# Kernel optimization log

Measured on AMD Instinct MI355X. Metric: run time of the kernel, lower is better.

## Reference

```python
import jax, jax.numpy as jnp
import numpy as np


def _lstm_dir(x, mask, Wi, Wh, b, reverse):
    """One direction of an LSTM layer with per-path length masking.
    x: [P,T,D], mask: [P,T] bool (True where t < length).
    Returns (outputs [P,T,H], final hidden [P,H]).
    State freezes outside the valid region, so the final carry equals the
    hidden state at the last valid step (fwd: t=len-1; bwd: t=0), matching
    torch's per-sequence LSTM on the unpadded sequence."""
    P, T, D = x.shape
    H = Wh.shape[1]
    xs = jnp.swapaxes(x, 0, 1)      # [T,P,D]
    ms = jnp.swapaxes(mask, 0, 1)   # [T,P]
    if reverse:
        xs, ms = xs[::-1], ms[::-1]
    h0 = jnp.zeros((P, H), x.dtype)

    def step(carry, inp):
        h, c = carry
        xt, mt = inp
        z = xt @ Wi.T + h @ Wh.T + b          # [P,4H], torch gate order i,f,g,o
        i, f, g, o = jnp.split(z, 4, axis=-1)
        c_new = jax.nn.sigmoid(f) * c + jax.nn.sigmoid(i) * jnp.tanh(g)
        h_new = jax.nn.sigmoid(o) * jnp.tanh(c_new)
        m = mt[:, None]
        h = jnp.where(m, h_new, h)
        c = jnp.where(m, c_new, c)
        return (h, c), h

    (h_fin, _), hs = jax.lax.scan(step, (h0, h0), (xs, ms))
    if reverse:
        hs = hs[::-1]
    return jnp.swapaxes(hs, 0, 1), h_fin


def setup_inputs() -> dict:
    key = jax.random.key(0)
    N, E, F, H, P, T = 50000, 256, 64, 256, 512, 256
    s = 0.05
    ks = jax.random.split(key, 24)
    d = {}
    d['sequences'] = jax.random.randint(ks[0], (P, T), 0, N)
    d['lengths'] = jax.random.randint(ks[1], (P,), 1, T + 1)  # >=1 so all paths valid
    d['features'] = jax.random.normal(ks[2], (P, F), jnp.float32)
    d['node_embeddings'] = jax.random.normal(ks[3], (N, E), jnp.float32)
    d['num_paths'] = P
    # node_projection
    d['Wp'] = jax.random.normal(ks[4], (H, E), jnp.float32) * s
    d['bp'] = jnp.zeros((H,), jnp.float32)
    # LSTM layer 0 (input H), fwd/rev; b = b_ih + b_hh folded together
    d['Wi0f'] = jax.random.normal(ks[5], (4 * H, H), jnp.float32) * s
    d['Wh0f'] = jax.random.normal(ks[6], (4 * H, H), jnp.float32) * s
    d['b0f'] = jnp.zeros((4 * H,), jnp.float32)
    d['Wi0r'] = jax.random.normal(ks[7], (4 * H, H), jnp.float32) * s
    d['Wh0r'] = jax.random.normal(ks[8], (4 * H, H), jnp.float32) * s
    d['b0r'] = jnp.zeros((4 * H,), jnp.float32)
    # LSTM layer 1 (input 2H), fwd/rev
    d['Wi1f'] = jax.random.normal(ks[9], (4 * H, 2 * H), jnp.float32) * s
    d['Wh1f'] = jax.random.normal(ks[10], (4 * H, H), jnp.float32) * s
    d['b1f'] = jnp.zeros((4 * H,), jnp.float32)
    d['Wi1r'] = jax.random.normal(ks[11], (4 * H, 2 * H), jnp.float32) * s
    d['Wh1r'] = jax.random.normal(ks[12], (4 * H, H), jnp.float32) * s
    d['b1r'] = jnp.zeros((4 * H,), jnp.float32)
    # feature_projection
    d['Wf'] = jax.random.normal(ks[13], (H, F), jnp.float32) * s
    d['bf'] = jnp.zeros((H,), jnp.float32)
    # path_fusion (3H -> H)
    d['Wfus'] = jax.random.normal(ks[14], (H, 3 * H), jnp.float32) * s
    d['bfus'] = jnp.zeros((H,), jnp.float32)
    # attention_projection (H -> 1)
    d['Wa'] = jax.random.normal(ks[15], (1, H), jnp.float32) * s
    d['ba'] = jnp.zeros((1,), jnp.float32)
    # aggregation_mlp: 3H -> 2H -> H
    d['W1'] = jax.random.normal(ks[16], (2 * H, 3 * H), jnp.float32) * s
    d['b1'] = jnp.zeros((2 * H,), jnp.float32)
    d['W2'] = jax.random.normal(ks[17], (H, 2 * H), jnp.float32) * s
    d['b2'] = jnp.zeros((H,), jnp.float32)
    return d


def reference(sequences, lengths, features, node_embeddings, num_paths,
              Wp, bp,
              Wi0f, Wh0f, b0f, Wi0r, Wh0r, b0r,
              Wi1f, Wh1f, b1f, Wi1r, Wh1r, b1r,
              Wf, bf, Wfus, bfus, Wa, ba, W1, b1, W2, b2):
    P, T = sequences.shape
    # gather + node projection (eval mode: dropout off)
    x = node_embeddings[sequences] @ Wp.T + bp               # [P,T,H]
    mask = jnp.arange(T)[None, :] < lengths[:, None]         # [P,T]
    # BiLSTM layer 0
    o0f, _ = _lstm_dir(x, mask, Wi0f, Wh0f, b0f, reverse=False)
    o0r, _ = _lstm_dir(x, mask, Wi0r, Wh0r, b0r, reverse=True)
    o0 = jnp.concatenate([o0f, o0r], axis=-1)                # [P,T,2H]
    # BiLSTM layer 1: only final hidden states needed (h_n[-2], h_n[-1])
    _, h1f = _lstm_dir(o0, mask, Wi1f, Wh1f, b1f, reverse=False)
    _, h1r = _lstm_dir(o0, mask, Wi1r, Wh1r, b1r, reverse=True)
    path_lstm = jnp.concatenate([h1f, h1r], axis=-1)         # [P,2H]
    path_feat = features @ Wf.T + bf                         # [P,H]
    combined = jnp.concatenate([path_lstm, path_feat], axis=-1)
    path_emb = jax.nn.relu(combined @ Wfus.T + bfus)         # [P,H]
    # attention pooling over paths
    attn = jax.nn.softmax(path_emb @ Wa.T + ba, axis=0)      # [P,1]
    weighted = (path_emb * attn).sum(axis=0, keepdims=True)  # [1,H]
    mean_p = path_emb.mean(axis=0, keepdims=True)
    max_p = path_emb.max(axis=0, keepdims=True)
    agg = jnp.concatenate([weighted, mean_p, max_p], axis=1)  # [1,3H]
    h = jax.nn.relu(agg @ W1.T + b1)
    return h @ W2.T + b2                                     # [1,H]
```

## Files before the change

kernel.cpp:

```cpp
#include <hip/hip_runtime.h>

typedef short bf8 __attribute__((ext_vector_type(8)));
typedef float f4  __attribute__((ext_vector_type(4)));
typedef int   i4  __attribute__((ext_vector_type(4)));

#define DEV static __device__ __forceinline__

DEV float bf2f(unsigned short u){ unsigned int x = ((unsigned int)u) << 16; float f; __builtin_memcpy(&f, &x, 4); return f; }
DEV unsigned short f2bf(float f){ unsigned int x; __builtin_memcpy(&x, &f, 4); unsigned int r = (x + 0x7fffu + ((x >> 16) & 1u)) >> 16; return (unsigned short)r; }
DEV float sigm(float z){ return 1.f / (1.f + __expf(-z)); }
DEV float tanh_fast(float z){ float e = __expf(2.f * z); return 1.f - 2.f / (e + 1.f); }

__global__ void k_cvt(const float* __restrict__ s, unsigned short* __restrict__ d, int n){
    int i = blockIdx.x * 256 + threadIdx.x;
    if (i < n) d[i] = f2bf(s[i]);
}

__global__ void k_cvt_t(const float* __restrict__ s, unsigned short* __restrict__ d){
    int e = blockIdx.x, h = threadIdx.x;
    d[e * 256 + h] = f2bf(s[h * 256 + e]);
}

__global__ void k_bias(const float* __restrict__ b0f, const float* __restrict__ Wi0f,
                       const float* __restrict__ b0r, const float* __restrict__ Wi0r,
                       const float* __restrict__ bp, float* __restrict__ bc){
    int g = blockIdx.x * 256 + threadIdx.x;
    const float* b = (g < 1024) ? b0f : b0r;
    const float* W = ((g < 1024) ? Wi0f : Wi0r) + (size_t)(g & 1023) * 256;
    float a = b[g & 1023];
    for (int k = 0; k < 256; ++k) a += W[k] * bp[k];
    bc[g] = a;
}

template<int K, int AMODE, bool OUTH>
__global__ __launch_bounds__(256)
void k_gemm(const unsigned short* __restrict__ A, const int* __restrict__ seq,
            const unsigned short* __restrict__ W, const float* __restrict__ bias,
            void* __restrict__ C, int N, int t0)
{
    __shared__ unsigned short Alds[128 * 32];
    __shared__ unsigned short Blds[128 * 32];
    const int tid = threadIdx.x, lane = tid & 63, wv = tid >> 6;
    const long m0 = (long)blockIdx.x * 128, n0 = (long)blockIdx.y * 128;

    const unsigned short* srcA[2]; const unsigned short* srcB[2]; int ldsOfs[2];
    #pragma unroll
    for (int q = 0; q < 2; ++q){
        int c = wv * 128 + q * 64 + lane;
        int r = c >> 2, kb = c & 3;
        int kg = kb ^ ((r >> 1) & 3);
        long m = m0 + r;
        long arow;
        if constexpr (AMODE == 0){
            arow = m;
        } else {
            long p = m >> 5; int ss = (int)(m & 31);
            int t = (AMODE == 2 || AMODE == 4) ? (t0 + ss) : (t0 - ss);
            arow = p * 256 + t;
            if constexpr (AMODE == 2 || AMODE == 3) arow = seq[arow];
        }
        srcA[q] = A + arow * K + kg * 8;
        srcB[q] = W + (n0 + r) * K + kg * 8;
        ldsOfs[q] = c * 8;
    }
    f4 acc[4][4] = {};
    const int ar = lane & 15, kq = lane >> 4;
    const int wm = (wv >> 1) * 64, wn = (wv & 1) * 64;

    for (int kk = 0; kk < K / 32; ++kk){
        i4 ra[2], rb[2];
        #pragma unroll
        for (int q = 0; q < 2; ++q){
            ra[q] = *(const i4*)(srcA[q] + kk * 32);
            rb[q] = *(const i4*)(srcB[q] + kk * 32);
        }
        __syncthreads();
        #pragma unroll
        for (int q = 0; q < 2; ++q){
            *(i4*)&Alds[ldsOfs[q]] = ra[q];
            *(i4*)&Blds[ldsOfs[q]] = rb[q];
        }
        __syncthreads();
        bf8 af[4], bfr[4];
        #pragma unroll
        for (int mt = 0; mt < 4; ++mt){
            int row = wm + mt * 16 + ar; int ph = kq ^ ((row >> 1) & 3);
            af[mt] = __builtin_bit_cast(bf8, *(const i4*)&Alds[row * 32 + ph * 8]);
        }
        #pragma unroll
        for (int nt = 0; nt < 4; ++nt){
            int row = wn + nt * 16 + ar; int ph = kq ^ ((row >> 1) & 3);
            bfr[nt] = __builtin_bit_cast(bf8, *(const i4*)&Blds[row * 32 + ph * 8]);
        }
        #pragma unroll
        for (int mt = 0; mt < 4; ++mt)
            #pragma unroll
            for (int nt = 0; nt < 4; ++nt)
                acc[mt][nt] = __builtin_amdgcn_mfma_f32_16x16x32_bf16(af[mt], bfr[nt], acc[mt][nt], 0, 0, 0);
    }
    #pragma unroll
    for (int nt = 0; nt < 4; ++nt){
        long n = n0 + wn + nt * 16 + ar;
        float bv = bias[n];
        #pragma unroll
        for (int mt = 0; mt < 4; ++mt){
            #pragma unroll
            for (int r = 0; r < 4; ++r){
                long m = m0 + wm + mt * 16 + kq * 4 + r;
                float v = acc[mt][nt][r] + bv;
                if (OUTH) ((_Float16*)C)[m * N + n] = (_Float16)v;
                else      ((unsigned short*)C)[m * N + n] = f2bf(v);
            }
        }
    }
}

template<int LAYER>
__global__ __launch_bounds__(256)
void k_step(int s, const unsigned short* __restrict__ Wh,
            const _Float16* __restrict__ zxF,
            const _Float16* __restrict__ zxR,
            unsigned short* __restrict__ o0,
            const unsigned short* __restrict__ hsR, unsigned short* __restrict__ hsW,
            float* __restrict__ cbuf,
            const int* __restrict__ lengths)
{
    __shared__ unsigned short Wlds[128 * 256];
    const int tid = threadIdx.x, lane = tid & 63, wv = tid >> 6;
    const int pt = blockIdx.x, jc = blockIdx.y, dir = blockIdx.z;
    const int t = dir ? 255 - s : s;
    const int tprev = dir ? t + 1 : t - 1;

    if (s > 0){
        for (int c = tid; c < 4096; c += 256){
            int r = c >> 5, kb = c & 31;
            int kg = kb ^ (r & 7);
            int wrow = (r >> 5) * 256 + jc * 32 + (r & 31);
            *(i4*)&Wlds[c * 8] = *(const i4*)&Wh[((size_t)(dir * 1024 + wrow)) * 256 + kg * 8];
        }
    }
    __syncthreads();

    const int ar = lane & 15, kq = lane >> 4;
    const int p0 = pt * 64 + wv * 16 + ar;
    f4 acc[8] = {};
    if (s > 0){
        bf8 af[8];
        const unsigned short* hp;
        if constexpr (LAYER == 0) hp = o0 + ((size_t)(p0 * 256 + tprev)) * 512 + dir * 256;
        else                      hp = hsR + ((size_t)(dir * 512 + p0)) * 256;
        #pragma unroll
        for (int k0 = 0; k0 < 8; ++k0)
            af[k0] = __builtin_bit_cast(bf8, *(const i4*)&hp[k0 * 32 + kq * 8]);
        #pragma unroll
        for (int nt = 0; nt < 8; ++nt){
            int row = nt * 16 + ar;
            #pragma unroll
            for (int k0 = 0; k0 < 8; ++k0){
                int ph = (k0 * 4 + kq) ^ (row & 7);
                bf8 b = __builtin_bit_cast(bf8, *(const i4*)&Wlds[row * 256 + ph * 8]);
                acc[nt] = __builtin_amdgcn_mfma_f32_16x16x32_bf16(af[k0], b, acc[nt], 0, 0, 0);
            }
        }
    }
    const _Float16* zb = dir ? zxR : zxF;
    const int ss = s & 31;
    #pragma unroll
    for (int sub = 0; sub < 2; ++sub){
        const int hcol = jc * 32 + sub * 16 + ar;
        #pragma unroll
        for (int r = 0; r < 4; ++r){
            const int path = pt * 64 + wv * 16 + kq * 4 + r;
            const size_t zofs = (((size_t)path << 5) + ss) * 1024 + hcol;
            float zi = acc[0 + sub][r] + (float)zb[zofs];
            float zf = acc[2 + sub][r] + (float)zb[zofs + 256];
            float zg = acc[4 + sub][r] + (float)zb[zofs + 512];
            float zo = acc[6 + sub][r] + (float)zb[zofs + 768];
            const bool m = t < lengths[path];
            float* cp = cbuf + ((size_t)(dir * 512 + path)) * 256 + hcol;
            float cold = *cp;
            float ig = sigm(zi), fg = sigm(zf), gg = tanh_fast(zg), og = sigm(zo);
            float cn = fg * cold + ig * gg;
            float hn = og * tanh_fast(cn);
            float hold = 0.f;
            if (s > 0){
                if constexpr (LAYER == 0) hold = bf2f(o0[((size_t)path * 256 + tprev) * 512 + dir * 256 + hcol]);
                else                      hold = bf2f(hsR[((size_t)(dir * 512 + path)) * 256 + hcol]);
            }
            if (m) *cp = cn;
            float ho = m ? hn : hold;
            if constexpr (LAYER == 0) o0[((size_t)path * 256 + t) * 512 + dir * 256 + hcol] = f2bf(ho);
            else                      hsW[((size_t)(dir * 512 + path)) * 256 + hcol] = f2bf(ho);
        }
    }
}

__global__ __launch_bounds__(256)
void k_fuse(const unsigned short* __restrict__ hsF,
            const float* __restrict__ features, const float* __restrict__ Wf, const float* __restrict__ bfv,
            const float* __restrict__ Wfus, const float* __restrict__ bfus,
            const float* __restrict__ Wa, const float* __restrict__ ba,
            float* __restrict__ pe, float* __restrict__ scores)
{
    __shared__ float comb[768];
    __shared__ float fl[64];
    __shared__ float red[256];
    const int p = blockIdx.x, tid = threadIdx.x;
    comb[tid]       = bf2f(hsF[(size_t)(0 * 512 + p) * 256 + tid]);
    comb[256 + tid] = bf2f(hsF[(size_t)(1 * 512 + p) * 256 + tid]);
    if (tid < 64) fl[tid] = features[p * 64 + tid];
    __syncthreads();
    float pf = bfv[tid];
    #pragma unroll 4
    for (int k = 0; k < 64; ++k) pf += fl[k] * Wf[tid * 64 + k];
    comb[512 + tid] = pf;
    __syncthreads();
    float a = bfus[tid];
    #pragma unroll 4
    for (int k = 0; k < 768; ++k) a += comb[k] * Wfus[tid * 768 + k];
    float pev = fmaxf(a, 0.f);
    pe[(size_t)p * 256 + tid] = pev;
    red[tid] = pev * Wa[tid];
    __syncthreads();
    for (int ofs = 128; ofs > 0; ofs >>= 1){
        if (tid < ofs) red[tid] += red[tid + ofs];
        __syncthreads();
    }
    if (tid == 0) scores[p] = red[0] + ba[0];
}

__global__ __launch_bounds__(512)
void k_head(const float* __restrict__ pe, const float* __restrict__ scores,
            const float* __restrict__ W1, const float* __restrict__ b1,
            const float* __restrict__ W2, const float* __restrict__ b2,
            float* __restrict__ out)
{
    __shared__ float att[512];
    __shared__ float red[512];
    __shared__ float agg[768];
    __shared__ float h1[512];
    const int tid = threadIdx.x;
    float s = scores[tid];
    red[tid] = s; __syncthreads();
    for (int ofs = 256; ofs > 0; ofs >>= 1){ if (tid < ofs) red[tid] = fmaxf(red[tid], red[tid + ofs]); __syncthreads(); }
    float mx = red[0]; __syncthreads();
    float e = __expf(s - mx);
    red[tid] = e; __syncthreads();
    for (int ofs = 256; ofs > 0; ofs >>= 1){ if (tid < ofs) red[tid] += red[tid + ofs]; __syncthreads(); }
    float sum = red[0]; __syncthreads();
    att[tid] = e / sum;
    __syncthreads();
    if (tid < 256){
        float w = 0.f, sm = 0.f, mxv = -1e30f;
        for (int p = 0; p < 512; ++p){
            float v = pe[(size_t)p * 256 + tid];
            w += att[p] * v; sm += v; mxv = fmaxf(mxv, v);
        }
        agg[tid] = w; agg[256 + tid] = sm * (1.f / 512.f); agg[512 + tid] = mxv;
    }
    __syncthreads();
    float hv = b1[tid];
    #pragma unroll 4
    for (int k = 0; k < 768; ++k) hv += agg[k] * W1[tid * 768 + k];
    hv = fmaxf(hv, 0.f);
    h1[tid] = hv;
    __syncthreads();
    if (tid < 256){
        float o = b2[tid];
        #pragma unroll 4
        for (int k = 0; k < 512; ++k) o += h1[k] * W2[tid * 512 + k];
        out[tid] = o;
    }
}

extern "C" void kernel_launch(void* const* d_in, const int* in_sizes, int n_in,
                              void* d_out, int out_size, void* d_ws, size_t ws_size,
                              hipStream_t stream)
{
    const int*   seq  = (const int*)  d_in[0];
    const int*   len  = (const int*)  d_in[1];
    const float* feat = (const float*)d_in[2];
    const float* emb  = (const float*)d_in[3];
    const float* Wp   = (const float*)d_in[5];
    const float* bp   = (const float*)d_in[6];
    const float* Wi0f = (const float*)d_in[7];
    const float* Wh0f = (const float*)d_in[8];
    const float* b0f  = (const float*)d_in[9];
    const float* Wi0r = (const float*)d_in[10];
    const float* Wh0r = (const float*)d_in[11];
    const float* b0r  = (const float*)d_in[12];
    const float* Wi1f = (const float*)d_in[13];
    const float* Wh1f = (const float*)d_in[14];
    const float* b1f  = (const float*)d_in[15];
    const float* Wi1r = (const float*)d_in[16];
    const float* Wh1r = (const float*)d_in[17];
    const float* b1r  = (const float*)d_in[18];
    const float* Wf   = (const float*)d_in[19];
    const float* bfv  = (const float*)d_in[20];
    const float* Wfus = (const float*)d_in[21];
    const float* bfus = (const float*)d_in[22];
    const float* Wa   = (const float*)d_in[23];
    const float* ba   = (const float*)d_in[24];
    const float* W1   = (const float*)d_in[25];
    const float* b1   = (const float*)d_in[26];
    const float* W2   = (const float*)d_in[27];
    const float* b2   = (const float*)d_in[28];

    char* ws = (char*)d_ws;
    size_t o = 0;
    auto alloc = [&](size_t bytes)->char*{ char* r = ws + o; o += (bytes + 255) & ~(size_t)255; return r; };

    unsigned short* emb_bf = (unsigned short*)alloc(50000UL * 256 * 2);
    unsigned short* wpT    = (unsigned short*)alloc(256UL * 256 * 2);
    unsigned short* wi0b   = (unsigned short*)alloc(2048UL * 256 * 2);
    unsigned short* wc0    = (unsigned short*)alloc(2048UL * 256 * 2);
    float*          bc0    = (float*)        alloc(2048UL * 4);
    float*          zbias  = (float*)        alloc(256UL * 4);
    unsigned short* wi1b   = (unsigned short*)alloc(2048UL * 512 * 2);
    unsigned short* wh0b   = (unsigned short*)alloc(2048UL * 256 * 2);
    unsigned short* wh1b   = (unsigned short*)alloc(2048UL * 256 * 2);
    unsigned short* o0p    = (unsigned short*)alloc(131072UL * 512 * 2);
    _Float16*       zxF    = (_Float16*)     alloc(512UL * 32 * 1024 * 2);
    _Float16*       zxR    = (_Float16*)     alloc(512UL * 32 * 1024 * 2);
    float*          c0p    = (float*)        alloc(2UL * 512 * 256 * 4);
    float*          c1p    = (float*)        alloc(2UL * 512 * 256 * 4);
    unsigned short* hsA    = (unsigned short*)alloc(2UL * 512 * 256 * 2);
    unsigned short* hsB    = (unsigned short*)alloc(2UL * 512 * 256 * 2);
    float*          pe     = (float*)        alloc(512UL * 256 * 4);
    float*          scores = (float*)        alloc(512UL * 4);
    (void)in_sizes; (void)n_in; (void)out_size;
    if (o > ws_size) return;

    auto cvt = [&](const float* s, unsigned short* d, int n){
        k_cvt<<<(n + 255) / 256, 256, 0, stream>>>(s, d, n);
    };
    cvt(emb,  emb_bf, 50000 * 256);
    k_cvt_t<<<256, 256, 0, stream>>>(Wp, wpT);
    cvt(Wi0f, wi0b,              1024 * 256);
    cvt(Wi0r, wi0b + 1024 * 256, 1024 * 256);
    cvt(Wh0f, wh0b,              1024 * 256);
    cvt(Wh0r, wh0b + 1024 * 256, 1024 * 256);
    cvt(Wi1f, wi1b,              1024 * 512);
    cvt(Wi1r, wi1b + 1024 * 512, 1024 * 512);
    cvt(Wh1f, wh1b,              1024 * 256);
    cvt(Wh1r, wh1b + 1024 * 256, 1024 * 256);
    k_bias<<<8, 256, 0, stream>>>(b0f, Wi0f, b0r, Wi0r, bp, bc0);
    hipMemsetAsync(zbias, 0, 256 * 4, stream);
    hipMemsetAsync(c0p, 0, 2UL * 512 * 256 * 4, stream);
    hipMemsetAsync(c1p, 0, 2UL * 512 * 256 * 4, stream);

    k_gemm<256, 0, false><<<dim3(16, 2), 256, 0, stream>>>(wi0b, nullptr, wpT, zbias, wc0, 256, 0);

    for (int c = 0; c < 8; ++c){
        int s0 = c * 32;
        k_gemm<256, 2, true><<<dim3(128, 8), 256, 0, stream>>>(emb_bf, seq, wc0,              bc0,        zxF, 1024, s0);
        k_gemm<256, 3, true><<<dim3(128, 8), 256, 0, stream>>>(emb_bf, seq, wc0 + 1024 * 256, bc0 + 1024, zxR, 1024, 255 - s0);
        for (int s = s0; s < s0 + 32; ++s)
            k_step<0><<<dim3(8, 8, 2), 256, 0, stream>>>(s, wh0b, zxF, zxR, o0p, nullptr, nullptr, c0p, len);
    }
    for (int c = 0; c < 8; ++c){
        int s0 = c * 32;
        k_gemm<512, 4, true><<<dim3(128, 8), 256, 0, stream>>>(o0p, nullptr, wi1b,              b1f, zxF, 1024, s0);
        k_gemm<512, 5, true><<<dim3(128, 8), 256, 0, stream>>>(o0p, nullptr, wi1b + 1024 * 512, b1r, zxR, 1024, 255 - s0);
        for (int s = s0; s < s0 + 32; ++s)
            k_step<1><<<dim3(8, 8, 2), 256, 0, stream>>>(s, wh1b, zxF, zxR, nullptr,
                (s & 1) ? hsA : hsB, (s & 1) ? hsB : hsA, c1p, len);
    }
    k_fuse<<<512, 256, 0, stream>>>(hsB, feat, Wf, bfv, Wfus, bfus, Wa, ba, pe, scores);
    k_head<<<1, 512, 0, stream>>>(pe, scores, W1, b1, W2, b2, (float*)d_out);
}
```

Baseline: 6.195 ms.

## Replace per-step LSTM launches with persistent kernels using flag-based cross-block sync

```diff
diff --git a/kernel.cpp b/kernel.cpp
--- a/kernel.cpp
+++ b/kernel.cpp
@@ -10,10 +10,16 @@
 DEV unsigned short f2bf(float f){ unsigned int x; __builtin_memcpy(&x, &f, 4); unsigned int r = (x + 0x7fffu + ((x >> 16) & 1u)) >> 16; return (unsigned short)r; }
 DEV float sigm(float z){ return 1.f / (1.f + __expf(-z)); }
 DEV float tanh_fast(float z){ float e = __expf(2.f * z); return 1.f - 2.f / (e + 1.f); }
+DEV bf8 ld16(const unsigned short* p){ return __builtin_bit_cast(bf8, *(const i4*)p); }
 
 __global__ void k_cvt(const float* __restrict__ s, unsigned short* __restrict__ d, int n){
     int i = blockIdx.x * 256 + threadIdx.x;
     if (i < n) d[i] = f2bf(s[i]);
+}
+
+__global__ void k_zero(unsigned int* __restrict__ d, int n){
+    int i = blockIdx.x * 256 + threadIdx.x;
+    if (i < n) d[i] = 0u;
 }
 
 __global__ void k_cvt_t(const float* __restrict__ s, unsigned short* __restrict__ d){
@@ -32,65 +38,46 @@
     bc[g] = a;
 }
 
-template<int K, int AMODE, bool OUTH>
 __global__ __launch_bounds__(256)
-void k_gemm(const unsigned short* __restrict__ A, const int* __restrict__ seq,
-            const unsigned short* __restrict__ W, const float* __restrict__ bias,
-            void* __restrict__ C, int N, int t0)
-{
+void k_gemm(const unsigned short* __restrict__ A, const unsigned short* __restrict__ W,
+            const float* __restrict__ bias, unsigned short* __restrict__ C, int N)
+{
+    const int K = 256;
     __shared__ unsigned short Alds[128 * 32];
     __shared__ unsigned short Blds[128 * 32];
     const int tid = threadIdx.x, lane = tid & 63, wv = tid >> 6;
     const long m0 = (long)blockIdx.x * 128, n0 = (long)blockIdx.y * 128;
-
     const unsigned short* srcA[2]; const unsigned short* srcB[2]; int ldsOfs[2];
     #pragma unroll
     for (int q = 0; q < 2; ++q){
         int c = wv * 128 + q * 64 + lane;
         int r = c >> 2, kb = c & 3;
         int kg = kb ^ ((r >> 1) & 3);
-        long m = m0 + r;
-        long arow;
-        if constexpr (AMODE == 0){
-            arow = m;
-        } else {
-            long p = m >> 5; int ss = (int)(m & 31);
-            int t = (AMODE == 2 || AMODE == 4) ? (t0 + ss) : (t0 - ss);
-            arow = p * 256 + t;
-            if constexpr (AMODE == 2 || AMODE == 3) arow = seq[arow];
-        }
-        srcA[q] = A + arow * K + kg * 8;
+        srcA[q] = A + (m0 + r) * K + kg * 8;
         srcB[q] = W + (n0 + r) * K + kg * 8;
         ldsOfs[q] = c * 8;
     }
     f4 acc[4][4] = {};
     const int ar = lane & 15, kq = lane >> 4;
     const int wm = (wv >> 1) * 64, wn = (wv & 1) * 64;
-
     for (int kk = 0; kk < K / 32; ++kk){
         i4 ra[2], rb[2];
         #pragma unroll
-        for (int q = 0; q < 2; ++q){
-            ra[q] = *(const i4*)(srcA[q] + kk * 32);
-            rb[q] = *(const i4*)(srcB[q] + kk * 32);
-        }
+        for (int q = 0; q < 2; ++q){ ra[q] = *(const i4*)(srcA[q] + kk * 32); rb[q] = *(const i4*)(srcB[q] + kk * 32); }
         __syncthreads();
         #pragma unroll
-        for (int q = 0; q < 2; ++q){
-            *(i4*)&Alds[ldsOfs[q]] = ra[q];
-            *(i4*)&Blds[ldsOfs[q]] = rb[q];
-        }
+        for (int q = 0; q < 2; ++q){ *(i4*)&Alds[ldsOfs[q]] = ra[q]; *(i4*)&Blds[ldsOfs[q]] = rb[q]; }
         __syncthreads();
         bf8 af[4], bfr[4];
         #pragma unroll
         for (int mt = 0; mt < 4; ++mt){
             int row = wm + mt * 16 + ar; int ph = kq ^ ((row >> 1) & 3);
-            af[mt] = __builtin_bit_cast(bf8, *(const i4*)&Alds[row * 32 + ph * 8]);
+            af[mt] = ld16(&Alds[row * 32 + ph * 8]);
         }
         #pragma unroll
         for (int nt = 0; nt < 4; ++nt){
             int row = wn + nt * 16 + ar; int ph = kq ^ ((row >> 1) & 3);
-            bfr[nt] = __builtin_bit_cast(bf8, *(const i4*)&Blds[row * 32 + ph * 8]);
+            bfr[nt] = ld16(&Blds[row * 32 + ph * 8]);
         }
         #pragma unroll
         for (int mt = 0; mt < 4; ++mt)
@@ -103,100 +90,146 @@
         long n = n0 + wn + nt * 16 + ar;
         float bv = bias[n];
         #pragma unroll
-        for (int mt = 0; mt < 4; ++mt){
+        for (int mt = 0; mt < 4; ++mt)
             #pragma unroll
             for (int r = 0; r < 4; ++r){
                 long m = m0 + wm + mt * 16 + kq * 4 + r;
-                float v = acc[mt][nt][r] + bv;
-                if (OUTH) ((_Float16*)C)[m * N + n] = (_Float16)v;
-                else      ((unsigned short*)C)[m * N + n] = f2bf(v);
-            }
-        }
+                C[m * N + n] = f2bf(acc[mt][nt][r] + bv);
+            }
     }
 }
 
 template<int LAYER>
+__global__ __launch_bounds__(256, 1)
+void k_persist(const unsigned short* __restrict__ Whw,
+               const unsigned short* __restrict__ Wxw,
+               const float* __restrict__ bias0,
+               const float* __restrict__ bias1,
+               const unsigned short* __restrict__ xsrc,
+               const int* __restrict__ seq,
+               const int* __restrict__ lengths,
+               unsigned short* __restrict__ o0,
+               unsigned short* __restrict__ hbuf,
+               unsigned int* __restrict__ flags)
+{
+    constexpr int XK = LAYER ? 512 : 256;
+    const int tid = threadIdx.x, lane = tid & 63, wv = tid >> 6;
+    const int b = blockIdx.x;
+    const int g = b & 15, jc = b >> 4;
+    const int pt = g >> 1, dir = g & 1;
+    const int ph = wv >> 1, gh = wv & 1;
+    const int pbase = pt * 64 + ph * 32;
+    const int hcbase = jc * 32 + gh * 16;
+    const int ar = lane & 15, kq = lane >> 4;
+    unsigned int* myflag = flags + g * 256;
+
+    bf8 whf[4][8], wxf[4][XK / 32];
+    #pragma unroll
+    for (int nt = 0; nt < 4; ++nt){
+        const int wrow = nt * 256 + hcbase + ar;
+        const unsigned short* wh = Whw + (size_t)(dir * 1024 + wrow) * 256 + kq * 8;
+        const unsigned short* wx = Wxw + (size_t)(dir * 1024 + wrow) * XK + kq * 8;
+        #pragma unroll
+        for (int k0 = 0; k0 < 8; ++k0) whf[nt][k0] = ld16(wh + k0 * 32);
+        #pragma unroll
+        for (int k0 = 0; k0 < XK / 32; ++k0) wxf[nt][k0] = ld16(wx + k0 * 32);
+    }
+    const int hcol = hcbase + ar;
+    const float* bb = dir ? bias1 : bias0;
+    const float bI = bb[hcol], bF = bb[256 + hcol], bG = bb[512 + hcol], bO = bb[768 + hcol];
+    int len_[2][4];
+    #pragma unroll
+    for (int mt = 0; mt < 2; ++mt)
+        #pragma unroll
+        for (int r = 0; r < 4; ++r) len_[mt][r] = lengths[pbase + mt * 16 + kq * 4 + r];
+    float cst[2][4] = {}, hst[2][4] = {};
+
+    for (int s = 0; s < 256; ++s){
+        const int t = dir ? 255 - s : s;
+        f4 acc[2][4] = {};
+        {
+            const unsigned short* xb[2];
+            #pragma unroll
+            for (int mt = 0; mt < 2; ++mt){
+                const int pa = pbase + mt * 16 + ar;
+                if constexpr (LAYER == 0){
+                    int e = seq[pa * 256 + t];
+                    xb[mt] = xsrc + (size_t)e * 256 + kq * 8;
+                } else {
+                    xb[mt] = xsrc + ((size_t)pa * 256 + t) * 512 + kq * 8;
+                }
+            }
+            #pragma unroll
+            for (int k0 = 0; k0 < XK / 32; ++k0){
+                bf8 a0 = ld16(xb[0] + k0 * 32);
+                bf8 a1 = ld16(xb[1] + k0 * 32);
+                #pragma unroll
+                for (int nt = 0; nt < 4; ++nt){
+                    acc[0][nt] = __builtin_amdgcn_mfma_f32_16x16x32_bf16(a0, wxf[nt][k0], acc[0][nt], 0, 0, 0);
+                    acc[1][nt] = __builtin_amdgcn_mfma_f32_16x16x32_bf16(a1, wxf[nt][k0], acc[1][nt], 0, 0, 0);
+                }
+            }
+        }
+        if (s > 0){
+            if (lane == 0){
+                unsigned int guard = 0;
+                while (__hip_atomic_load(myflag + (s - 1), __ATOMIC_ACQUIRE, __HIP_MEMORY_SCOPE_SYSTEM) < 8u){
+                    if (++guard > 2000000u) break;
+                    __builtin_amdgcn_s_sleep(1);
+                }
+            }
+            __syncthreads();
+            __threadfence();
+            const int tprev = dir ? t + 1 : t - 1;
+            const unsigned short* hb[2];
+            #pragma unroll
+            for (int mt = 0; mt < 2; ++mt){
+                const int pa = pbase + mt * 16 + ar;
+                if constexpr (LAYER == 0)
+                    hb[mt] = o0 + ((size_t)pa * 256 + tprev) * 512 + dir * 256 + kq * 8;
+                else
+                    hb[mt] = hbuf + ((size_t)((dir * 2 + ((s - 1) & 1)) * 512) + pa) * 256 + kq * 8;
+            }
+            #pragma unroll
+            for (int k0 = 0; k0 < 8; ++k0){
+                bf8 a0 = ld16(hb[0] + k0 * 32);
+                bf8 a1 = ld16(hb[1] + k0 * 32);
+                #pragma unroll
+                for (int nt = 0; nt < 4; ++nt){
+                    acc[0][nt] = __builtin_amdgcn_mfma_f32_16x16x32_bf16(a0, whf[nt][k0], acc[0][nt], 0, 0, 0);
+                    acc[1][nt] = __builtin_amdgcn_mfma_f32_16x16x32_bf16(a1, whf[nt][k0], acc[1][nt], 0, 0, 0);
+                }
+            }
+        }
+        #pragma unroll
+        for (int mt = 0; mt < 2; ++mt){
+            #pragma unroll
+            for (int r = 0; r < 4; ++r){
+                float zi = acc[mt][0][r] + bI;
+                float zf = acc[mt][1][r] + bF;
+                float zg = acc[mt][2][r] + bG;
+                float zo = acc[mt][3][r] + bO;
+                const int pa = pbase + mt * 16 + kq * 4 + r;
+                const bool m = t < len_[mt][r];
+                float cn = sigm(zf) * cst[mt][r] + sigm(zi) * tanh_fast(zg);
+                float hn = sigm(zo) * tanh_fast(cn);
+                if (m){ cst[mt][r] = cn; hst[mt][r] = hn; }
+                const unsigned short hb16 = f2bf(hst[mt][r]);
+                if constexpr (LAYER == 0)
+                    o0[((size_t)pa * 256 + t) * 512 + dir * 256 + hcol] = hb16;
+                else
+                    hbuf[((size_t)((dir * 2 + (s & 1)) * 512) + pa) * 256 + hcol] = hb16;
+            }
+        }
+        __threadfence();
+        __syncthreads();
+        if (tid == 0)
+            __hip_atomic_fetch_add(myflag + s, 1u, __ATOMIC_RELEASE, __HIP_MEMORY_SCOPE_SYSTEM);
+    }
+}
+
 __global__ __launch_bounds__(256)
-void k_step(int s, const unsigned short* __restrict__ Wh,
-            const _Float16* __restrict__ zxF,
-            const _Float16* __restrict__ zxR,
-            unsigned short* __restrict__ o0,
-            const unsigned short* __restrict__ hsR, unsigned short* __restrict__ hsW,
-            float* __restrict__ cbuf,
-            const int* __restrict__ lengths)
-{
-    __shared__ unsigned short Wlds[128 * 256];
-    const int tid = threadIdx.x, lane = tid & 63, wv = tid >> 6;
-    const int pt = blockIdx.x, jc = blockIdx.y, dir = blockIdx.z;
-    const int t = dir ? 255 - s : s;
-    const int tprev = dir ? t + 1 : t - 1;
-
-    if (s > 0){
-        for (int c = tid; c < 4096; c += 256){
-            int r = c >> 5, kb = c & 31;
-            int kg = kb ^ (r & 7);
-            int wrow = (r >> 5) * 256 + jc * 32 + (r & 31);
-            *(i4*)&Wlds[c * 8] = *(const i4*)&Wh[((size_t)(dir * 1024 + wrow)) * 256 + kg * 8];
-        }
-    }
-    __syncthreads();
-
-    const int ar = lane & 15, kq = lane >> 4;
-    const int p0 = pt * 64 + wv * 16 + ar;
-    f4 acc[8] = {};
-    if (s > 0){
-        bf8 af[8];
-        const unsigned short* hp;
-        if constexpr (LAYER == 0) hp = o0 + ((size_t)(p0 * 256 + tprev)) * 512 + dir * 256;
-        else                      hp = hsR + ((size_t)(dir * 512 + p0)) * 256;
-        #pragma unroll
-        for (int k0 = 0; k0 < 8; ++k0)
-            af[k0] = __builtin_bit_cast(bf8, *(const i4*)&hp[k0 * 32 + kq * 8]);
-        #pragma unroll
-        for (int nt = 0; nt < 8; ++nt){
-            int row = nt * 16 + ar;
-            #pragma unroll
-            for (int k0 = 0; k0 < 8; ++k0){
-                int ph = (k0 * 4 + kq) ^ (row & 7);
-                bf8 b = __builtin_bit_cast(bf8, *(const i4*)&Wlds[row * 256 + ph * 8]);
-                acc[nt] = __builtin_amdgcn_mfma_f32_16x16x32_bf16(af[k0], b, acc[nt], 0, 0, 0);
-            }
-        }
-    }
-    const _Float16* zb = dir ? zxR : zxF;
-    const int ss = s & 31;
-    #pragma unroll
-    for (int sub = 0; sub < 2; ++sub){
-        const int hcol = jc * 32 + sub * 16 + ar;
-        #pragma unroll
-        for (int r = 0; r < 4; ++r){
-            const int path = pt * 64 + wv * 16 + kq * 4 + r;
-            const size_t zofs = (((size_t)path << 5) + ss) * 1024 + hcol;
-            float zi = acc[0 + sub][r] + (float)zb[zofs];
-            float zf = acc[2 + sub][r] + (float)zb[zofs + 256];
-            float zg = acc[4 + sub][r] + (float)zb[zofs + 512];
-            float zo = acc[6 + sub][r] + (float)zb[zofs + 768];
-            const bool m = t < lengths[path];
-            float* cp = cbuf + ((size_t)(dir * 512 + path)) * 256 + hcol;
-            float cold = *cp;
-            float ig = sigm(zi), fg = sigm(zf), gg = tanh_fast(zg), og = sigm(zo);
-            float cn = fg * cold + ig * gg;
-            float hn = og * tanh_fast(cn);
-            float hold = 0.f;
-            if (s > 0){
-                if constexpr (LAYER == 0) hold = bf2f(o0[((size_t)path * 256 + tprev) * 512 + dir * 256 + hcol]);
-                else                      hold = bf2f(hsR[((size_t)(dir * 512 + path)) * 256 + hcol]);
-            }
-            if (m) *cp = cn;
-            float ho = m ? hn : hold;
-            if constexpr (LAYER == 0) o0[((size_t)path * 256 + t) * 512 + dir * 256 + hcol] = f2bf(ho);
-            else                      hsW[((size_t)(dir * 512 + path)) * 256 + hcol] = f2bf(ho);
-        }
-    }
-}
-
-__global__ __launch_bounds__(256)
-void k_fuse(const unsigned short* __restrict__ hsF,
+void k_fuse(const unsigned short* __restrict__ hbuf,
             const float* __restrict__ features, const float* __restrict__ Wf, const float* __restrict__ bfv,
             const float* __restrict__ Wfus, const float* __restrict__ bfus,
             const float* __restrict__ Wa, const float* __restrict__ ba,
@@ -206,8 +239,8 @@
     __shared__ float fl[64];
     __shared__ float red[256];
     const int p = blockIdx.x, tid = threadIdx.x;
-    comb[tid]       = bf2f(hsF[(size_t)(0 * 512 + p) * 256 + tid]);
-    comb[256 + tid] = bf2f(hsF[(size_t)(1 * 512 + p) * 256 + tid]);
+    comb[tid]       = bf2f(hbuf[((size_t)(0 * 2 + 1) * 512 + p) * 256 + tid]);
+    comb[256 + tid] = bf2f(hbuf[((size_t)(1 * 2 + 1) * 512 + p) * 256 + tid]);
     if (tid < 64) fl[tid] = features[p * 64 + tid];
     __syncthreads();
     float pf = bfv[tid];
@@ -320,12 +353,9 @@
     unsigned short* wh0b   = (unsigned short*)alloc(2048UL * 256 * 2);
     unsigned short* wh1b   = (unsigned short*)alloc(2048UL * 256 * 2);
     unsigned short* o0p    = (unsigned short*)alloc(131072UL * 512 * 2);
-    _Float16*       zxF    = (_Float16*)     alloc(512UL * 32 * 1024 * 2);
-    _Float16*       zxR    = (_Float16*)     alloc(512UL * 32 * 1024 * 2);
-    float*          c0p    = (float*)        alloc(2UL * 512 * 256 * 4);
-    float*          c1p    = (float*)        alloc(2UL * 512 * 256 * 4);
-    unsigned short* hsA    = (unsigned short*)alloc(2UL * 512 * 256 * 2);
-    unsigned short* hsB    = (unsigned short*)alloc(2UL * 512 * 256 * 2);
+    unsigned short* hbuf   = (unsigned short*)alloc(4UL * 512 * 256 * 2);
+    unsigned int*   flags0 = (unsigned int*) alloc(16UL * 256 * 4);
+    unsigned int*   flags1 = (unsigned int*) alloc(16UL * 256 * 4);
     float*          pe     = (float*)        alloc(512UL * 256 * 4);
     float*          scores = (float*)        alloc(512UL * 4);
     (void)in_sizes; (void)n_in; (void)out_size;
@@ -345,27 +375,15 @@
     cvt(Wh1f, wh1b,              1024 * 256);
     cvt(Wh1r, wh1b + 1024 * 256, 1024 * 256);
     k_bias<<<8, 256, 0, stream>>>(b0f, Wi0f, b0r, Wi0r, bp, bc0);
-    hipMemsetAsync(zbias, 0, 256 * 4, stream);
-    hipMemsetAsync(c0p, 0, 2UL * 512 * 256 * 4, stream);
-    hipMemsetAsync(c1p, 0, 2UL * 512 * 256 * 4, stream);
-
-    k_gemm<256, 0, false><<<dim3(16, 2), 256, 0, stream>>>(wi0b, nullptr, wpT, zbias, wc0, 256, 0);
-
-    for (int c = 0; c < 8; ++c){
-        int s0 = c * 32;
-        k_gemm<256, 2, true><<<dim3(128, 8), 256, 0, stream>>>(emb_bf, seq, wc0,              bc0,        zxF, 1024, s0);
-        k_gemm<256, 3, true><<<dim3(128, 8), 256, 0, stream>>>(emb_bf, seq, wc0 + 1024 * 256, bc0 + 1024, zxR, 1024, 255 - s0);
-        for (int s = s0; s < s0 + 32; ++s)
-            k_step<0><<<dim3(8, 8, 2), 256, 0, stream>>>(s, wh0b, zxF, zxR, o0p, nullptr, nullptr, c0p, len);
-    }
-    for (int c = 0; c < 8; ++c){
-        int s0 = c * 32;
-        k_gemm<512, 4, true><<<dim3(128, 8), 256, 0, stream>>>(o0p, nullptr, wi1b,              b1f, zxF, 1024, s0);
-        k_gemm<512, 5, true><<<dim3(128, 8), 256, 0, stream>>>(o0p, nullptr, wi1b + 1024 * 512, b1r, zxR, 1024, 255 - s0);
-        for (int s = s0; s < s0 + 32; ++s)
-            k_step<1><<<dim3(8, 8, 2), 256, 0, stream>>>(s, wh1b, zxF, zxR, nullptr,
-                (s & 1) ? hsA : hsB, (s & 1) ? hsB : hsA, c1p, len);
-    }
-    k_fuse<<<512, 256, 0, stream>>>(hsB, feat, Wf, bfv, Wfus, bfus, Wa, ba, pe, scores);
+    k_zero<<<32, 256, 0, stream>>>(flags0, 16 * 256 * 2);
+    k_zero<<<1, 256, 0, stream>>>((unsigned int*)zbias, 256);
+
+    k_gemm<<<dim3(16, 2), 256, 0, stream>>>(wi0b, wpT, zbias, wc0, 256);
+
+    k_persist<0><<<128, 256, 0, stream>>>(wh0b, wc0, bc0, bc0 + 1024, emb_bf, seq, len,
+                                          o0p, nullptr, flags0);
+    k_persist<1><<<128, 256, 0, stream>>>(wh1b, wi1b, b1f, b1r, o0p, nullptr, len,
+                                          nullptr, hbuf, flags1);
+    k_fuse<<<512, 256, 0, stream>>>(hbuf, feat, Wf, bfv, Wfus, bfus, Wa, ba, pe, scores);
     k_head<<<1, 512, 0, stream>>>(pe, scores, W1, b1, W2, b2, (float*)d_out);
 }
```

After: 16.87 ms. 2.72x slower.
